# Kernel tuning notes

Measured on AMD Instinct MI355X. Metric: run time of the kernel, lower is better.

Reference implementation:

```python
import jax, jax.numpy as jnp
import numpy as np

B, S, H, NH, HD = 4, 2048, 2048, 16, 128
SCALE = HD ** -0.5


def rotate_half(x):
    x1, x2 = jnp.split(x, 2, axis=-1)
    return jnp.concatenate([-x2, x1], axis=-1)


def setup_inputs() -> dict:
    key = jax.random.key(0)
    ks = jax.random.split(key, 8)
    x = jax.random.normal(ks[0], (B, S, H), dtype=jnp.float32)
    # RoPE tables for positions 0..S-1, standard theta=10000 construction
    inv_freq = 1.0 / (10000.0 ** (jnp.arange(0, HD, 2, dtype=jnp.float32) / HD))
    t = jnp.arange(S, dtype=jnp.float32)
    freqs = jnp.einsum('s,d->sd', t, inv_freq)          # [S, HD/2]
    emb = jnp.concatenate([freqs, freqs], axis=-1)      # [S, HD]
    cos, sin = jnp.cos(emb), jnp.sin(emb)
    # causal mask: True = masked (future positions)
    mask = jnp.triu(jnp.ones((S, S), dtype=bool), k=1)
    std = H ** -0.5
    Wq = jax.random.normal(ks[1], (H, H), dtype=jnp.float32) * std
    Wk = jax.random.normal(ks[2], (H, H), dtype=jnp.float32) * std
    Wv = jax.random.normal(ks[3], (H, H), dtype=jnp.float32) * std
    Wo = jax.random.normal(ks[4], (H, H), dtype=jnp.float32) * std
    return {"x": x, "cos": cos, "sin": sin, "mask": mask,
            "Wq": Wq, "Wk": Wk, "Wv": Wv, "Wo": Wo}


def reference(x, cos, sin, mask, Wq, Wk, Wv, Wo):
    # projections: nn.Linear(bias=False) => x @ W.T
    def proj(W):
        y = jnp.einsum('bsh,ih->bsi', x, W)             # [B,S,inner]
        return y.reshape(B, S, NH, HD).transpose(0, 2, 1, 3)  # [B,NH,S,HD]
    q, k, v = proj(Wq), proj(Wk), proj(Wv)
    # RoPE (rotate-half), cos/sin broadcast over batch & heads
    c = cos[None, None, :, :]
    s = sin[None, None, :, :]
    q = q * c + rotate_half(q) * s
    k = k * c + rotate_half(k) * s
    # attention
    attn = jnp.einsum('bhqd,bhkd->bhqk', q, k) * SCALE
    attn = jnp.where(mask[None, None, :, :], -jnp.inf, attn)
    attn = jax.nn.softmax(attn, axis=-1)
    out = jnp.einsum('bhqk,bhkd->bhqd', attn, v)
    out = out.transpose(0, 2, 1, 3).reshape(B, S, NH * HD)
    y = jnp.einsum('bsi,hi->bsh', out, Wo)
    return y, k, v
```

## Files before the change

kernel.cpp:

```cpp
#include <hip/hip_runtime.h>
#include <hip/hip_bf16.h>
#include <math.h>

typedef __bf16 bf16_t;
typedef __bf16 bf16x8 __attribute__((ext_vector_type(8)));
typedef __bf16 bf16x4v __attribute__((ext_vector_type(4)));
typedef float  f32x4  __attribute__((ext_vector_type(4)));
typedef float  f32x16 __attribute__((ext_vector_type(16)));
typedef unsigned int u32x4 __attribute__((ext_vector_type(4)));

constexpr int CB = 4, CS = 2048, CH = 2048, CNH = 16, CHD = 128;
constexpr int CM = CB * CS;
constexpr float CSCALE = 0.08838834764831845f;
constexpr float CL2E   = 1.4426950408889634f;
constexpr float CSC2   = CSCALE * CL2E;

__device__ __forceinline__ float fexp2(float x) {
  float r;
  asm("v_exp_f32 %0, %1" : "=v"(r) : "v"(x));
  return r;
}

__device__ __forceinline__ void g2l16(const void* g, void* l) {
  __builtin_amdgcn_global_load_lds(
      (const __attribute__((address_space(1))) void*)g,
      (__attribute__((address_space(3))) void*)l, 16, 0, 0);
}

__global__ __launch_bounds__(256) void cvt_all(const float* __restrict__ x,
                                               const float* __restrict__ Wq,
                                               const float* __restrict__ Wk,
                                               const float* __restrict__ Wv,
                                               const float* __restrict__ Wo,
                                               bf16_t* __restrict__ xb,
                                               bf16_t* __restrict__ wqb,
                                               bf16_t* __restrict__ wkb,
                                               bf16_t* __restrict__ wvb,
                                               bf16_t* __restrict__ wob) {
  constexpr int NX = CM * CH / 4;
  constexpr int NW = CH * CH / 4;
  const int i = blockIdx.x * 256 + threadIdx.x;
  const float* src;
  bf16_t* dst;
  int off;
  if (i < NX) {
    src = x; dst = xb; off = i;
  } else {
    const int j = i - NX;
    const int sel = j / NW;
    off = j - sel * NW;
    src = (sel == 0) ? Wq : (sel == 1) ? Wk : (sel == 2) ? Wv : Wo;
    dst = (sel == 0) ? wqb : (sel == 1) ? wkb : (sel == 2) ? wvb : wob;
  }
  float4 v = reinterpret_cast<const float4*>(src)[off];
  bf16x4v o = {(bf16_t)v.x, (bf16_t)v.y, (bf16_t)v.z, (bf16_t)v.w};
  reinterpret_cast<bf16x4v*>(dst)[off] = o;
}

__device__ __forceinline__ void gemm256sq_core(const bf16_t* __restrict__ A,
                                               const bf16_t* __restrict__ Bm,
                                               bf16_t (*As2)[4][64 * 64],
                                               bf16_t (*Bs2)[4][64 * 64],
                                               int row0, int col0,
                                               f32x4 (&acc)[8][4]) {
  const int tid = threadIdx.x, lane = tid & 63, w = tid >> 6;
  const int wm = w >> 2, wn = w & 3;
  constexpr int NKT = CH / 64;
  const int id = w * 64 + lane;
  const int rl = id >> 3, ck = id & 7;

  auto stA = [&](int buf, int kt, int q) {
    const int row = q * 64 + rl;
    g2l16(A + (size_t)(row0 + row) * CH + kt * 64 + ((ck ^ (row & 7)) << 3),
          &As2[buf][q][id * 8]);
  };
  auto stB = [&](int buf, int kt, int q) {
    const int row = q * 64 + rl;
    g2l16(Bm + (size_t)(col0 + row) * CH + kt * 64 + ((ck ^ (row & 7)) << 3),
          &Bs2[buf][q][id * 8]);
  };
  auto rdA = [&](int buf, int r, int c) -> bf16x8 {
    return *(const bf16x8*)(&As2[buf][r >> 6][(r & 63) * 64 + ((c ^ (r & 7)) << 3)]);
  };
  auto rdB = [&](int buf, int r, int c) -> bf16x8 {
    return *(const bf16x8*)(&Bs2[buf][r >> 6][(r & 63) * 64 + ((c ^ (r & 7)) << 3)]);
  };

#pragma unroll
  for (int q = 0; q < 4; ++q) stB(0, 0, q);
#pragma unroll
  for (int q = 0; q < 4; ++q) stA(0, 0, q);
  asm volatile("s_waitcnt vmcnt(0)" ::: "memory");
  __builtin_amdgcn_s_barrier();
  __builtin_amdgcn_sched_barrier(0);

  const int ar0 = wm * 128 + (lane & 15);
  const int br0 = wn * 64 + (lane & 15);
  const int chi = lane >> 4;

  for (int t = 0; t < NKT; ++t) {
    const int buf = t & 1, nbuf = buf ^ 1;
    const bool pf = (t + 1 < NKT);
    bf16x8 bb[4][2], aa[2][2];

#pragma unroll
    for (int p = 0; p < 4; ++p) {
      if (p == 0) {
#pragma unroll
        for (int nf = 0; nf < 4; ++nf)
#pragma unroll
          for (int kk = 0; kk < 2; ++kk)
            bb[nf][kk] = rdB(buf, br0 + nf * 16, kk * 4 + chi);
      }
#pragma unroll
      for (int i = 0; i < 2; ++i)
#pragma unroll
        for (int kk = 0; kk < 2; ++kk)
          aa[i][kk] = rdA(buf, ar0 + (2 * p + i) * 16, kk * 4 + chi);

      if (pf) {
        if (p == 0) { stB(nbuf, t + 1, 0); stB(nbuf, t + 1, 1); }
        if (p == 1) { stB(nbuf, t + 1, 2); stB(nbuf, t + 1, 3); }
        if (p == 2) { stA(nbuf, t + 1, 0); stA(nbuf, t + 1, 2); }
        if (p == 3) { stA(nbuf, t + 1, 1); stA(nbuf, t + 1, 3); }
      }

      __builtin_amdgcn_s_barrier();
      asm volatile("s_waitcnt lgkmcnt(0)" ::: "memory");
      __builtin_amdgcn_sched_barrier(0);
      __builtin_amdgcn_s_setprio(1);
#pragma unroll
      for (int i = 0; i < 2; ++i)
#pragma unroll
        for (int nf = 0; nf < 4; ++nf)
#pragma unroll
          for (int kk = 0; kk < 2; ++kk)
            acc[2 * p + i][nf] = __builtin_amdgcn_mfma_f32_16x16x32_bf16(
                aa[i][kk], bb[nf][kk], acc[2 * p + i][nf], 0, 0, 0);
      __builtin_amdgcn_s_setprio(0);

      if (p == 1) {
        if (pf) { asm volatile("s_waitcnt vmcnt(4)" ::: "memory"); }
        else    { asm volatile("s_waitcnt vmcnt(0)" ::: "memory"); }
      }
      if (p == 3 && pf) { asm volatile("s_waitcnt vmcnt(2)" ::: "memory"); }
      __builtin_amdgcn_s_barrier();
      __builtin_amdgcn_sched_barrier(0);
    }
  }
}

__global__ __launch_bounds__(512, 1) void qkv_gemm(const bf16_t* __restrict__ xb,
                                                   const bf16_t* __restrict__ wqb,
                                                   const bf16_t* __restrict__ wkb,
                                                   const bf16_t* __restrict__ wvb,
                                                   const float* __restrict__ cosd,
                                                   const float* __restrict__ sind,
                                                   bf16_t* __restrict__ qraw,
                                                   bf16_t* __restrict__ knat,
                                                   bf16_t* __restrict__ vt2,
                                                   float* __restrict__ kout,
                                                   float* __restrict__ vout) {
  __shared__ __align__(16) bf16_t LSD[2][2][4][64 * 64];
  const int z = blockIdx.z;
  const bf16_t* Bm = (z == 0) ? wqb : ((z == 1) ? wkb : wvb);
  const int row0 = blockIdx.x * 256, col0 = blockIdx.y * 256;
  f32x4 acc[8][4] = {};
  gemm256sq_core(xb, Bm, LSD[0], LSD[1], row0, col0, acc);

  const int tid = threadIdx.x, lane = tid & 63, w = tid >> 6;
  const int wm = w >> 2, wn = w & 3;

  if (z == 2) {
#pragma unroll
    for (int i = 0; i < 8; ++i) {
#pragma unroll
      for (int j = 0; j < 4; ++j) {
        const int gr0 = row0 + wm * 128 + i * 16 + (lane >> 4) * 4;
        const int gc = col0 + wn * 64 + j * 16 + (lane & 15);
        const int b = gr0 >> 11, s0 = gr0 & (CS - 1);
        const int nh = gc >> 7, hd = gc & (CHD - 1);
        const int bh = b * CNH + nh;
#pragma unroll
        for (int r = 0; r < 4; ++r) {
          const size_t idx = ((size_t)bh * CS + s0 + r) * CHD + hd;
          vout[idx] = acc[i][j][r];
        }
        bf16x4v pv = {(bf16_t)acc[i][j][0], (bf16_t)acc[i][j][1],
                      (bf16_t)acc[i][j][2], (bf16_t)acc[i][j][3]};
        *(bf16x4v*)(vt2 + (((size_t)bh * (CS / 16) + (s0 >> 4)) * CHD + hd) * 16 +
                    (s0 & 15)) = pv;
      }
    }
    return;
  }

  bf16_t* L = &LSD[0][0][0][0];
#pragma unroll
  for (int i = 0; i < 8; ++i)
#pragma unroll
    for (int j = 0; j < 4; ++j) {
      const int col = wn * 64 + j * 16 + (lane & 15);
#pragma unroll
      for (int r = 0; r < 4; ++r) {
        const int row = wm * 128 + i * 16 + (lane >> 4) * 4 + r;
        L[row * 256 + (((col >> 3) ^ (row & 31)) << 3) + (col & 7)] =
            (bf16_t)acc[i][j][r];
      }
    }
  __syncthreads();

  if (z == 0) {
#pragma unroll
    for (int k = 0; k < 16; ++k) {
      const int u = k * 512 + tid;
      const int row = u >> 5, ch = u & 31;
      bf16x8 v = *(const bf16x8*)&L[row * 256 + ((ch ^ (row & 31)) << 3)];
      const int gr = row0 + row, gc = col0 + ch * 8;
      const int b = gr >> 11, s = gr & (CS - 1), nh = gc >> 7, hd = gc & (CHD - 1);
      *(bf16x8*)&qraw[((size_t)(b * CNH + nh) * CS + s) * CHD + hd] = v;
    }
  } else {
#pragma unroll
    for (int k = 0; k < 16; ++k) {
      const int u = k * 512 + tid;
      const int row = u >> 5, ch = u & 31;
      bf16x8 v = *(const bf16x8*)&L[row * 256 + ((ch ^ (row & 31)) << 3)];
      bf16x8 p = *(const bf16x8*)&L[row * 256 + (((ch ^ 8) ^ (row & 31)) << 3)];
      const int gr = row0 + row, gc = col0 + ch * 8;
      const int b = gr >> 11, s = gr & (CS - 1), nh = gc >> 7, hd = gc & (CHD - 1);
      const float sgn = (hd < 64) ? -1.f : 1.f;
      float c[8], sn[8], o[8];
      *(float4*)(c)      = *(const float4*)(cosd + (size_t)s * CHD + hd);
      *(float4*)(c + 4)  = *(const float4*)(cosd + (size_t)s * CHD + hd + 4);
      *(float4*)(sn)     = *(const float4*)(sind + (size_t)s * CHD + hd);
      *(float4*)(sn + 4) = *(const float4*)(sind + (size_t)s * CHD + hd + 4);
#pragma unroll
      for (int e = 0; e < 8; ++e)
        o[e] = (float)v[e] * c[e] + sgn * (float)p[e] * sn[e];
      float* kp = kout + ((size_t)(b * CNH + nh) * CS + s) * CHD + hd;
      *(float4*)(kp)     = *(float4*)(o);
      *(float4*)(kp + 4) = *(float4*)(o + 4);
    }
#pragma unroll
    for (int k = 0; k < 16; ++k) {
      const int u = k * 512 + tid;
      const int s = u & 255, cc = u >> 8;
      bf16x8 v = *(const bf16x8*)&L[s * 256 + ((cc ^ (s & 31)) << 3)];
      bf16x8 p = *(const bf16x8*)&L[s * 256 + (((cc ^ 8) ^ (s & 31)) << 3)];
      const int gr = row0 + s, gc = col0 + cc * 8;
      const int b = gr >> 11, sg = gr & (CS - 1), nh = gc >> 7, hd = gc & (CHD - 1);
      const float sgn = (hd < 64) ? -1.f : 1.f;
      float c[8], sn[8];
      *(float4*)(c)      = *(const float4*)(cosd + (size_t)sg * CHD + hd);
      *(float4*)(c + 4)  = *(const float4*)(cosd + (size_t)sg * CHD + hd + 4);
      *(float4*)(sn)     = *(const float4*)(sind + (size_t)sg * CHD + hd);
      *(float4*)(sn + 4) = *(const float4*)(sind + (size_t)sg * CHD + hd + 4);
      bf16x8 o;
#pragma unroll
      for (int e = 0; e < 8; ++e)
        o[e] = (bf16_t)((float)v[e] * c[e] + sgn * (float)p[e] * sn[e]);
      const int pan = hd >> 4, half = (hd >> 3) & 1;
      *(bf16x8*)&knat[(((size_t)(b * CNH + nh) * 8 + pan) * CS + sg) * 16 +
                      half * 8] = o;
    }
  }
}

__global__ __launch_bounds__(512, 1) void y_gemm(const bf16_t* __restrict__ ob,
                                                 const bf16_t* __restrict__ wob,
                                                 float* __restrict__ yout) {
  __shared__ __align__(16) bf16_t As2[2][4][64 * 64];
  __shared__ __align__(16) bf16_t Bs2[2][4][64 * 64];
  const int row0 = blockIdx.x * 256, col0 = blockIdx.y * 256;
  f32x4 acc[8][4] = {};
  gemm256sq_core(ob, wob, As2, Bs2, row0, col0, acc);
  const int lane = threadIdx.x & 63, w = threadIdx.x >> 6;
  const int wm = w >> 2, wn = w & 3;
#pragma unroll
  for (int i = 0; i < 8; ++i)
#pragma unroll
    for (int j = 0; j < 4; ++j)
#pragma unroll
      for (int r = 0; r < 4; ++r) {
        const int gr = row0 + wm * 128 + i * 16 + (lane >> 4) * 4 + r;
        const int gc = col0 + wn * 64 + j * 16 + (lane & 15);
        yout[(size_t)gr * CH + gc] = acc[i][j][r];
      }
}

__global__ __launch_bounds__(128) void attn_kernel(const bf16_t* __restrict__ qb,
                                                   const bf16_t* __restrict__ kn,
                                                   const bf16_t* __restrict__ v2,
                                                   const float* __restrict__ cosd,
                                                   const float* __restrict__ sind,
                                                   bf16_t* __restrict__ ob) {
  __shared__ float Os[32][129];
  __shared__ float Ms[32], Ls[32];
  const int tid = threadIdx.x, lane = tid & 63, wh = tid >> 6;
  const int hi = lane >> 5, l31 = lane & 31;

  const int swz = (blockIdx.x & 7) * 512 + (blockIdx.x >> 3);
  const int bh = swz >> 6;
  const int qt = 63 - (swz & 63);

  const int b = bh >> 4, nh = bh & (CNH - 1);
  const bf16_t* kbase = kn + (size_t)bh * 8 * CS * 16;
  const bf16_t* vbase = v2 + (size_t)bh * (CS / 16) * CHD * 16;
  const int qw0 = qt * 32;
  const int qrow = qw0 + l31;

  bf16x8 bq[8];
  {
    const bf16_t* qp = qb + ((size_t)bh * CS + qrow) * CHD + hi * 8;
    bf16x8 raw[8];
#pragma unroll
    for (int ks = 0; ks < 8; ++ks) raw[ks] = *(const bf16x8*)(qp + ks * 16);
#pragma unroll
    for (int p = 0; p < 4; ++p) {
      const int d0 = p * 16 + hi * 8;
      float cc[8], ss[8];
      *(float4*)(cc)     = *(const float4*)(cosd + (size_t)qrow * CHD + d0);
      *(float4*)(cc + 4) = *(const float4*)(cosd + (size_t)qrow * CHD + d0 + 4);
      *(float4*)(ss)     = *(const float4*)(sind + (size_t)qrow * CHD + d0);
      *(float4*)(ss + 4) = *(const float4*)(sind + (size_t)qrow * CHD + d0 + 4);
#pragma unroll
      for (int e = 0; e < 8; ++e) {
        const float x1 = (float)raw[p][e], x2 = (float)raw[p + 4][e];
        bq[p][e]     = (bf16_t)(x1 * cc[e] - x2 * ss[e]);
        bq[p + 4][e] = (bf16_t)(x2 * cc[e] + x1 * ss[e]);
      }
    }
  }

  float m_ = -INFINITY, l_ = 0.f;
  f32x16 o_[4] = {};

  const int nt = (qt >> 1) + 1;
  for (int kt = wh; kt < nt; kt += 2) {
    const int kvb = kt * 64;

    bf16x8 ak[2][8];
#pragma unroll
    for (int kb2 = 0; kb2 < 2; ++kb2) {
      const bf16_t* kr = kbase + (size_t)(kvb + kb2 * 32 + l31) * 16 + hi * 8;
#pragma unroll
      for (int ks = 0; ks < 8; ++ks)
        ak[kb2][ks] = *(const bf16x8*)(kr + (size_t)ks * CS * 16);
    }

    f32x16 st[2] = {};
#pragma unroll
    for (int kb2 = 0; kb2 < 2; ++kb2)
#pragma unroll
      for (int ks = 0; ks < 8; ++ks)
        st[kb2] = __builtin_amdgcn_mfma_f32_32x32x16_bf16(ak[kb2][ks], bq[ks],
                                                          st[kb2], 0, 0, 0);

    bf16x8 av[4][4];
#pragma unroll
    for (int hb = 0; hb < 4; ++hb) {
      const bf16_t* vr = vbase + ((size_t)(kvb >> 4) * CHD + hb * 32 + l31) * 16 + hi * 8;
#pragma unroll
      for (int ks = 0; ks < 4; ++ks)
        av[hb][ks] = *(const bf16x8*)(vr + (size_t)ks * CHD * 16);
    }

    const bool anymask = (kvb + 63) > qw0;
#pragma unroll
    for (int blk = 0; blk < 2; ++blk)
#pragma unroll
      for (int r = 0; r < 16; ++r) {
        float xv = st[blk][r] * CSC2;
        if (anymask) {
          const int kv = kvb + blk * 32 + 4 * hi + (r & 3) + 8 * (r >> 2);
          if (kv > qrow) xv = -INFINITY;
        }
        st[blk][r] = xv;
      }

    float tmax = st[0][0];
#pragma unroll
    for (int r = 1; r < 16; ++r) tmax = fmaxf(tmax, st[0][r]);
#pragma unroll
    for (int r = 0; r < 16; ++r) tmax = fmaxf(tmax, st[1][r]);
    tmax = fmaxf(tmax, __shfl_xor(tmax, 32, 64));

    if (__any(tmax - m_ > 8.0f)) {
      const float mn = fmaxf(m_, tmax);
      const float corr = fexp2(m_ - mn);
      m_ = mn;
      l_ *= corr;
#pragma unroll
      for (int hb = 0; hb < 4; ++hb) o_[hb] *= corr;
    }

    float psum = 0.f;
#pragma unroll
    for (int blk = 0; blk < 2; ++blk)
#pragma unroll
      for (int r = 0; r < 16; ++r) {
        const float pv = fexp2(st[blk][r] - m_);
        st[blk][r] = pv;
        psum += pv;
      }
    psum += __shfl_xor(psum, 32, 64);
    l_ += psum;

    bf16x8 pb[4];
#pragma unroll
    for (int ks = 0; ks < 4; ++ks) {
      const int blk = ks >> 1, r0 = (ks & 1) * 8;
      unsigned pw0, pw1, pw2, pw3;
      asm("v_cvt_pk_bf16_f32 %0, %1, %2" : "=v"(pw0) : "v"(st[blk][r0 + 0]), "v"(st[blk][r0 + 1]));
      asm("v_cvt_pk_bf16_f32 %0, %1, %2" : "=v"(pw2) : "v"(st[blk][r0 + 4]), "v"(st[blk][r0 + 5]));
      asm("v_cvt_pk_bf16_f32 %0, %1, %2" : "=v"(pw1) : "v"(st[blk][r0 + 2]), "v"(st[blk][r0 + 3]));
      asm("v_cvt_pk_bf16_f32 %0, %1, %2" : "=v"(pw3) : "v"(st[blk][r0 + 6]), "v"(st[blk][r0 + 7]));
      asm("v_permlane32_swap_b32 %0, %1" : "+v"(pw0), "+v"(pw2));
      asm("v_permlane32_swap_b32 %0, %1" : "+v"(pw1), "+v"(pw3));
      u32x4 pk = {pw0, pw1, pw2, pw3};
      pb[ks] = *reinterpret_cast<bf16x8*>(&pk);
    }

#pragma unroll
    for (int hb = 0; hb < 4; ++hb)
#pragma unroll
      for (int ks = 0; ks < 4; ++ks)
        o_[hb] = __builtin_amdgcn_mfma_f32_32x32x16_bf16(av[hb][ks], pb[ks],
                                                         o_[hb], 0, 0, 0);
  }

  if (wh == 1) {
#pragma unroll
    for (int hb = 0; hb < 4; ++hb)
#pragma unroll
      for (int r = 0; r < 16; ++r) {
        const int hd = 32 * hb + 4 * hi + (r & 3) + 8 * (r >> 2);
        Os[l31][hd] = o_[hb][r];
      }
    if (hi == 0) { Ms[l31] = m_; Ls[l31] = l_; }
  }
  __builtin_amdgcn_s_barrier();
  if (wh == 1) return;

  const float m1 = Ms[l31], l1 = Ls[l31];
  const float mn = fmaxf(m_, m1);
  const float c0 = fexp2(m_ - mn), c1 = fexp2(m1 - mn);
  const float linv = 1.0f / (l_ * c0 + l1 * c1);
  bf16_t* orow = ob + ((size_t)(b * CS + qrow)) * CH + nh * CHD;
#pragma unroll
  for (int hb = 0; hb < 4; ++hb)
#pragma unroll
    for (int g = 0; g < 4; ++g) {
      const int hd0 = 32 * hb + 4 * hi + 8 * g;
      bf16x4v pv = {
          (bf16_t)((o_[hb][4 * g + 0] * c0 + Os[l31][hd0 + 0] * c1) * linv),
          (bf16_t)((o_[hb][4 * g + 1] * c0 + Os[l31][hd0 + 1] * c1) * linv),
          (bf16_t)((o_[hb][4 * g + 2] * c0 + Os[l31][hd0 + 2] * c1) * linv),
          (bf16_t)((o_[hb][4 * g + 3] * c0 + Os[l31][hd0 + 3] * c1) * linv)};
      *(bf16x4v*)(orow + hd0) = pv;
    }
}

extern "C" void kernel_launch(void* const* d_in, const int* in_sizes, int n_in,
                              void* d_out, int out_size, void* d_ws, size_t ws_size,
                              hipStream_t stream) {
  const float* x    = (const float*)d_in[0];
  const float* cosd = (const float*)d_in[1];
  const float* sind = (const float*)d_in[2];
  const float* Wq = (const float*)d_in[4];
  const float* Wk = (const float*)d_in[5];
  const float* Wv = (const float*)d_in[6];
  const float* Wo = (const float*)d_in[7];

  float* yout = (float*)d_out;
  float* kout = yout + (size_t)CM * CH;
  float* vout = kout + (size_t)CM * CH;

  char* ws = (char*)d_ws;
  size_t off = 0;
  auto wsalloc = [&](size_t bytes) {
    void* p = ws + off;
    off += (bytes + 255) & ~(size_t)255;
    return p;
  };
  bf16_t* xb   = (bf16_t*)wsalloc((size_t)CM * CH * 2);
  bf16_t* wqb  = (bf16_t*)wsalloc((size_t)CH * CH * 2);
  bf16_t* wkb  = (bf16_t*)wsalloc((size_t)CH * CH * 2);
  bf16_t* wvb  = (bf16_t*)wsalloc((size_t)CH * CH * 2);
  bf16_t* wob  = (bf16_t*)wsalloc((size_t)CH * CH * 2);
  bf16_t* qraw = (bf16_t*)wsalloc((size_t)CM * CH * 2);
  bf16_t* knat = (bf16_t*)wsalloc((size_t)CM * CH * 2);
  bf16_t* vt2  = (bf16_t*)wsalloc((size_t)CM * CH * 2);
  bf16_t* ob   = (bf16_t*)wsalloc((size_t)CM * CH * 2);

  cvt_all<<<(CM * CH / 4 + 4 * CH * CH / 4) / 256, 256, 0, stream>>>(
      x, Wq, Wk, Wv, Wo, xb, wqb, wkb, wvb, wob);

  qkv_gemm<<<dim3(CM / 256, CH / 256, 3), 512, 0, stream>>>(
      xb, wqb, wkb, wvb, cosd, sind, qraw, knat, vt2, kout, vout);
  attn_kernel<<<CB * CNH * (CS / 32), 128, 0, stream>>>(qraw, knat, vt2, cosd,
                                                        sind, ob);
  y_gemm<<<dim3(CM / 256, CH / 256), 512, 0, stream>>>(ob, wob, yout);
}
```

Measured before the change: 506.2 us.

## Stage GEMM epilogues through LDS for coalesced vector stores of V and Y

The V-projection epilogue now writes the bf16 tile to swizzled LDS and reads it back row-contiguous, so the fp32 V output goes out as float4 stores instead of scattered scalar stores. The y_gemm epilogue similarly stages fp32 accumulators through LDS in two halves and writes Y with coalesced float4 stores. The prefetch order of A and B sub-tiles inside the GEMM main loop is also reshuffled. The fp32 V output is now rounded through bf16 before being written, which loses precision relative to the previous exact fp32 store. The extra barriers and LDS round trips add latency in exchange for better global write coalescing.

```diff
diff --git a/kernel.cpp b/kernel.cpp
--- a/kernel.cpp
+++ b/kernel.cpp
@@ -120,8 +120,8 @@
 
       if (pf) {
         if (p == 0) { stB(nbuf, t + 1, 0); stB(nbuf, t + 1, 1); }
-        if (p == 1) { stB(nbuf, t + 1, 2); stB(nbuf, t + 1, 3); }
-        if (p == 2) { stA(nbuf, t + 1, 0); stA(nbuf, t + 1, 2); }
+        if (p == 1) { stA(nbuf, t + 1, 0); stA(nbuf, t + 1, 2); }
+        if (p == 2) { stB(nbuf, t + 1, 2); stB(nbuf, t + 1, 3); }
         if (p == 3) { stA(nbuf, t + 1, 1); stA(nbuf, t + 1, 3); }
       }
 
@@ -171,9 +171,22 @@
   const int tid = threadIdx.x, lane = tid & 63, w = tid >> 6;
   const int wm = w >> 2, wn = w & 3;
 
+  bf16_t* L = &LSD[0][0][0][0];
+#pragma unroll
+  for (int i = 0; i < 8; ++i)
+#pragma unroll
+    for (int j = 0; j < 4; ++j) {
+      const int col = wn * 64 + j * 16 + (lane & 15);
+#pragma unroll
+      for (int r = 0; r < 4; ++r) {
+        const int row = wm * 128 + i * 16 + (lane >> 4) * 4 + r;
+        L[row * 256 + (((col >> 3) ^ (row & 31)) << 3) + (col & 7)] =
+            (bf16_t)acc[i][j][r];
+      }
+    }
   if (z == 2) {
 #pragma unroll
-    for (int i = 0; i < 8; ++i) {
+    for (int i = 0; i < 8; ++i)
 #pragma unroll
       for (int j = 0; j < 4; ++j) {
         const int gr0 = row0 + wm * 128 + i * 16 + (lane >> 4) * 4;
@@ -181,33 +194,12 @@
         const int b = gr0 >> 11, s0 = gr0 & (CS - 1);
         const int nh = gc >> 7, hd = gc & (CHD - 1);
         const int bh = b * CNH + nh;
-#pragma unroll
-        for (int r = 0; r < 4; ++r) {
-          const size_t idx = ((size_t)bh * CS + s0 + r) * CHD + hd;
-          vout[idx] = acc[i][j][r];
-        }
         bf16x4v pv = {(bf16_t)acc[i][j][0], (bf16_t)acc[i][j][1],
                       (bf16_t)acc[i][j][2], (bf16_t)acc[i][j][3]};
         *(bf16x4v*)(vt2 + (((size_t)bh * (CS / 16) + (s0 >> 4)) * CHD + hd) * 16 +
                     (s0 & 15)) = pv;
       }
-    }
-    return;
-  }
-
-  bf16_t* L = &LSD[0][0][0][0];
-#pragma unroll
-  for (int i = 0; i < 8; ++i)
-#pragma unroll
-    for (int j = 0; j < 4; ++j) {
-      const int col = wn * 64 + j * 16 + (lane & 15);
-#pragma unroll
-      for (int r = 0; r < 4; ++r) {
-        const int row = wm * 128 + i * 16 + (lane >> 4) * 4 + r;
-        L[row * 256 + (((col >> 3) ^ (row & 31)) << 3) + (col & 7)] =
-            (bf16_t)acc[i][j][r];
-      }
-    }
+  }
   __syncthreads();
 
   if (z == 0) {
@@ -219,6 +211,21 @@
       const int gr = row0 + row, gc = col0 + ch * 8;
       const int b = gr >> 11, s = gr & (CS - 1), nh = gc >> 7, hd = gc & (CHD - 1);
       *(bf16x8*)&qraw[((size_t)(b * CNH + nh) * CS + s) * CHD + hd] = v;
+    }
+  } else if (z == 2) {
+#pragma unroll
+    for (int k = 0; k < 16; ++k) {
+      const int u = k * 512 + tid;
+      const int row = u >> 5, ch = u & 31;
+      bf16x8 v = *(const bf16x8*)&L[row * 256 + ((ch ^ (row & 31)) << 3)];
+      const int gr = row0 + row, gc = col0 + ch * 8;
+      const int b = gr >> 11, s = gr & (CS - 1), nh = gc >> 7, hd = gc & (CHD - 1);
+      float o[8];
+#pragma unroll
+      for (int e = 0; e < 8; ++e) o[e] = (float)v[e];
+      float* vp = vout + ((size_t)(b * CNH + nh) * CS + s) * CHD + hd;
+      *(float4*)(vp)     = *(float4*)(o);
+      *(float4*)(vp + 4) = *(float4*)(o + 4);
     }
   } else {
 #pragma unroll
@@ -270,23 +277,40 @@
 __global__ __launch_bounds__(512, 1) void y_gemm(const bf16_t* __restrict__ ob,
                                                  const bf16_t* __restrict__ wob,
                                                  float* __restrict__ yout) {
-  __shared__ __align__(16) bf16_t As2[2][4][64 * 64];
-  __shared__ __align__(16) bf16_t Bs2[2][4][64 * 64];
+  __shared__ __align__(16) bf16_t LSD[2][2][4][64 * 64];
   const int row0 = blockIdx.x * 256, col0 = blockIdx.y * 256;
   f32x4 acc[8][4] = {};
-  gemm256sq_core(ob, wob, As2, Bs2, row0, col0, acc);
-  const int lane = threadIdx.x & 63, w = threadIdx.x >> 6;
+  gemm256sq_core(ob, wob, LSD[0], LSD[1], row0, col0, acc);
+  const int tid = threadIdx.x, lane = tid & 63, w = tid >> 6;
   const int wm = w >> 2, wn = w & 3;
-#pragma unroll
-  for (int i = 0; i < 8; ++i)
-#pragma unroll
-    for (int j = 0; j < 4; ++j)
-#pragma unroll
-      for (int r = 0; r < 4; ++r) {
-        const int gr = row0 + wm * 128 + i * 16 + (lane >> 4) * 4 + r;
-        const int gc = col0 + wn * 64 + j * 16 + (lane & 15);
-        yout[(size_t)gr * CH + gc] = acc[i][j][r];
-      }
+  float* Lf = (float*)&LSD[0][0][0][0];
+
+#pragma unroll
+  for (int half = 0; half < 2; ++half) {
+    if (wm == half) {
+#pragma unroll
+      for (int i = 0; i < 8; ++i)
+#pragma unroll
+        for (int j = 0; j < 4; ++j) {
+          const int col = wn * 64 + j * 16 + (lane & 15);
+#pragma unroll
+          for (int r = 0; r < 4; ++r) {
+            const int rl = i * 16 + (lane >> 4) * 4 + r;
+            Lf[rl * 256 + col] = acc[i][j][r];
+          }
+        }
+    }
+    __syncthreads();
+#pragma unroll
+    for (int k = 0; k < 16; ++k) {
+      const int u = k * 512 + tid;
+      const int rl = u >> 6, ch = u & 63;
+      float4 v = *(const float4*)&Lf[rl * 256 + ch * 4];
+      const int gr = row0 + half * 128 + rl, gc = col0 + ch * 4;
+      *(float4*)&yout[(size_t)gr * CH + gc] = v;
+    }
+    __syncthreads();
+  }
 }
 
 __global__ __launch_bounds__(128) void attn_kernel(const bf16_t* __restrict__ qb,
```

Result: no change. 505.6 us (-0.1%).
